# Optimization experiments

Measured on AMD Instinct MI355X. Metric: run time of the kernel, lower is better.

## Reference

```python
import jax, jax.numpy as jnp
import numpy as np

K = 32
TEMPERATURE = 0.1
RTOL, ATOL = 1e-5, 1e-5


def _embed(x, W1, b1, W2, b2, W3, b3):
    h = jax.nn.gelu(x @ W1.T + b1, approximate=False)
    h = jax.nn.gelu(h @ W2.T + b2, approximate=False)
    return jax.nn.sigmoid(h @ W3.T + b3)


def setup_inputs() -> dict:
    key = jax.random.key(0)
    ks = jax.random.split(key, 9)
    Q, N, D_IN, D_E = 256, 16384, 256, 64
    s = lambda fan_in: 1.0 / np.sqrt(fan_in)
    return {
        "x": jax.random.normal(ks[0], (Q, D_IN), jnp.float32),
        "support_x": jax.random.normal(ks[1], (N, D_IN), jnp.float32),
        "support_labels": jax.random.uniform(ks[2], (N, 1), jnp.float32),
        "W1": jax.random.normal(ks[3], (D_E, D_IN), jnp.float32) * s(D_IN),
        "b1": jax.random.normal(ks[4], (D_E,), jnp.float32) * s(D_IN),
        "W2": jax.random.normal(ks[5], (D_E, D_E), jnp.float32) * s(D_E),
        "b2": jax.random.normal(ks[6], (D_E,), jnp.float32) * s(D_E),
        "W3": jax.random.normal(ks[7], (D_E, D_E), jnp.float32) * s(D_E),
        "b3": jax.random.normal(ks[8], (D_E,), jnp.float32) * s(D_E),
    }


def reference(x, support_x, support_labels, W1, b1, W2, b2, W3, b3):
    # query embeddings [Q, D]; support embeddings [N, D] (set_support is no_grad)
    q = _embed(x, W1, b1, W2, b2, W3, b3)
    s = jax.lax.stop_gradient(_embed(support_x, W1, b1, W2, b2, W3, b3))
    # torch.cdist p=2 via expanded squared distances
    d2 = (jnp.sum(q * q, -1)[:, None] + jnp.sum(s * s, -1)[None, :]
          - 2.0 * (q @ s.T))
    dist = jnp.sqrt(jnp.maximum(d2, 0.0))  # [Q, N]
    # isclose mask: |q - s| <= atol + rtol*|s|, all over feature dim
    close = jnp.abs(q[:, None, :] - s[None, :, :]) <= (ATOL + RTOL * jnp.abs(s)[None, :, :])
    mask = jnp.all(close, axis=-1)  # [Q, N]
    dist = jnp.where(mask, jnp.inf, dist)
    # top-k smallest distances
    neg_top, idx = jax.lax.top_k(-dist, K)  # [Q, K]
    topd = -neg_top
    neighbor_labels = support_labels[idx].squeeze(-1)  # [Q, K]
    weights = jax.nn.softmax(-topd / TEMPERATURE, axis=1)
    return jnp.sum(weights * neighbor_labels, axis=1)  # [Q]
```

## Files before the change

kernel.cpp:

```cpp
#include <hip/hip_runtime.h>
#include <math.h>

#define D_IN   256
#define D_E    64
#define N_SUP  16384
#define NQ     256
#define KSEL   32
#define RTOLC  1e-5f
#define ATOLC  1e-5f
#define INV_T  10.0f

#define CHUNK  1024
#define NCH    16
#define QG     16
#define NQG    16

typedef unsigned long long ull;

__device__ __forceinline__ float gelu_exact(float x) {
    return 0.5f * x * (1.0f + erff(x * 0.70710678118654752440f));
}

__global__ __launch_bounds__(256, 2) void embed_kernel(
    const float* __restrict__ sx, const float* __restrict__ x,
    const float* __restrict__ W1, const float* __restrict__ b1,
    const float* __restrict__ W2, const float* __restrict__ b2,
    const float* __restrict__ W3, const float* __restrict__ b3,
    float* __restrict__ s_emb, float* __restrict__ s_norm,
    float* __restrict__ q_emb, float* __restrict__ q_norm)
{
    __shared__ float xc[2][64][68];
    __shared__ float wc[2][64][68];
    __shared__ float nsq[64][17];

    const int tid = threadIdx.x;
    const int rg  = tid >> 4;
    const int fg  = tid & 15;
    const bool isq = blockIdx.x >= (N_SUP / 64);
    const int rowbase = isq ? (int)(blockIdx.x - N_SUP / 64) * 64
                            : (int)blockIdx.x * 64;
    const float* src = (isq ? x : sx) + (size_t)rowbase * D_IN;

    #define STAGE_X(kc_, b_)                                                   \
        {                                                                      \
            _Pragma("unroll")                                                  \
            for (int i_ = 0; i_ < 4; ++i_) {                                   \
                int g_ = i_ * 256 + tid;                                       \
                int row_ = g_ >> 4, c4_ = g_ & 15;                             \
                float4 v_ = *reinterpret_cast<const float4*>(                  \
                    src + (size_t)row_ * D_IN + (kc_) * 64 + c4_ * 4);         \
                xc[b_][c4_ * 4 + 0][row_] = v_.x;                              \
                xc[b_][c4_ * 4 + 1][row_] = v_.y;                              \
                xc[b_][c4_ * 4 + 2][row_] = v_.z;                              \
                xc[b_][c4_ * 4 + 3][row_] = v_.w;                              \
            }                                                                  \
        }
    #define STAGE_W1(kc_, b_)                                                  \
        {                                                                      \
            _Pragma("unroll")                                                  \
            for (int i_ = 0; i_ < 4; ++i_) {                                   \
                int g_ = i_ * 256 + tid;                                       \
                int f_ = g_ >> 4, c4_ = g_ & 15;                               \
                float4 w_ = *reinterpret_cast<const float4*>(                  \
                    W1 + (size_t)f_ * D_IN + (kc_) * 64 + c4_ * 4);            \
                wc[b_][c4_ * 4 + 0][f_] = w_.x;                                \
                wc[b_][c4_ * 4 + 1][f_] = w_.y;                                \
                wc[b_][c4_ * 4 + 2][f_] = w_.z;                                \
                wc[b_][c4_ * 4 + 3][f_] = w_.w;                                \
            }                                                                  \
        }
    #define STAGE_WSQ(Wp_, b_)                                                 \
        {                                                                      \
            _Pragma("unroll")                                                  \
            for (int i_ = 0; i_ < 4; ++i_) {                                   \
                int g_ = i_ * 256 + tid;                                       \
                int f_ = g_ >> 4, c4_ = g_ & 15;                               \
                float4 w_ = *reinterpret_cast<const float4*>(                  \
                    (Wp_) + (size_t)f_ * D_E + c4_ * 4);                       \
                wc[b_][c4_ * 4 + 0][f_] = w_.x;                                \
                wc[b_][c4_ * 4 + 1][f_] = w_.y;                                \
                wc[b_][c4_ * 4 + 2][f_] = w_.z;                                \
                wc[b_][c4_ * 4 + 3][f_] = w_.w;                                \
            }                                                                  \
        }
    #define GEMM64(XB_, WB_, ACC_)                                             \
        {                                                                      \
            _Pragma("unroll 8")                                                \
            for (int k_ = 0; k_ < 64; ++k_) {                                  \
                float4 xv_ = *reinterpret_cast<const float4*>(&XB_[k_][rg * 4]); \
                float4 wv_ = *reinterpret_cast<const float4*>(&WB_[k_][fg * 4]); \
                ACC_[0][0] = fmaf(wv_.x, xv_.x, ACC_[0][0]);                   \
                ACC_[0][1] = fmaf(wv_.y, xv_.x, ACC_[0][1]);                   \
                ACC_[0][2] = fmaf(wv_.z, xv_.x, ACC_[0][2]);                   \
                ACC_[0][3] = fmaf(wv_.w, xv_.x, ACC_[0][3]);                   \
                ACC_[1][0] = fmaf(wv_.x, xv_.y, ACC_[1][0]);                   \
                ACC_[1][1] = fmaf(wv_.y, xv_.y, ACC_[1][1]);                   \
                ACC_[1][2] = fmaf(wv_.z, xv_.y, ACC_[1][2]);                   \
                ACC_[1][3] = fmaf(wv_.w, xv_.y, ACC_[1][3]);                   \
                ACC_[2][0] = fmaf(wv_.x, xv_.z, ACC_[2][0]);                   \
                ACC_[2][1] = fmaf(wv_.y, xv_.z, ACC_[2][1]);                   \
                ACC_[2][2] = fmaf(wv_.z, xv_.z, ACC_[2][2]);                   \
                ACC_[2][3] = fmaf(wv_.w, xv_.z, ACC_[2][3]);                   \
                ACC_[3][0] = fmaf(wv_.x, xv_.w, ACC_[3][0]);                   \
                ACC_[3][1] = fmaf(wv_.y, xv_.w, ACC_[3][1]);                   \
                ACC_[3][2] = fmaf(wv_.z, xv_.w, ACC_[3][2]);                   \
                ACC_[3][3] = fmaf(wv_.w, xv_.w, ACC_[3][3]);                   \
            }                                                                  \
        }

    float4 bv1 = *reinterpret_cast<const float4*>(b1 + fg * 4);
    float acc[4][4];
    #pragma unroll
    for (int j = 0; j < 4; ++j) {
        acc[j][0] = bv1.x; acc[j][1] = bv1.y; acc[j][2] = bv1.z; acc[j][3] = bv1.w;
    }
    STAGE_X(0, 0); STAGE_W1(0, 0);
    __syncthreads();
    #pragma unroll
    for (int kc = 0; kc < 4; ++kc) {
        const int b = kc & 1;
        if (kc < 3) { STAGE_X(kc + 1, b ^ 1); STAGE_W1(kc + 1, b ^ 1); }
        GEMM64(xc[b], wc[b], acc);
        __syncthreads();
    }

    #pragma unroll
    for (int j = 0; j < 4; ++j)
        #pragma unroll
        for (int i = 0; i < 4; ++i)
            xc[0][fg * 4 + i][rg * 4 + j] = gelu_exact(acc[j][i]);
    STAGE_WSQ(W2, 0);
    STAGE_WSQ(W3, 1);
    __syncthreads();

    float4 bv2 = *reinterpret_cast<const float4*>(b2 + fg * 4);
    float a2[4][4];
    #pragma unroll
    for (int j = 0; j < 4; ++j) {
        a2[j][0] = bv2.x; a2[j][1] = bv2.y; a2[j][2] = bv2.z; a2[j][3] = bv2.w;
    }
    GEMM64(xc[0], wc[0], a2);
    __syncthreads();
    #pragma unroll
    for (int j = 0; j < 4; ++j)
        #pragma unroll
        for (int i = 0; i < 4; ++i)
            xc[1][fg * 4 + i][rg * 4 + j] = gelu_exact(a2[j][i]);
    __syncthreads();

    float4 bv3 = *reinterpret_cast<const float4*>(b3 + fg * 4);
    float a3[4][4];
    #pragma unroll
    for (int j = 0; j < 4; ++j) {
        a3[j][0] = bv3.x; a3[j][1] = bv3.y; a3[j][2] = bv3.z; a3[j][3] = bv3.w;
    }
    GEMM64(xc[1], wc[1], a3);

    float* E   = isq ? q_emb  : s_emb;
    float* Nrm = isq ? q_norm : s_norm;
    #pragma unroll
    for (int j = 0; j < 4; ++j) {
        float e0 = 1.0f / (1.0f + expf(-a3[j][0]));
        float e1 = 1.0f / (1.0f + expf(-a3[j][1]));
        float e2 = 1.0f / (1.0f + expf(-a3[j][2]));
        float e3 = 1.0f / (1.0f + expf(-a3[j][3]));
        *reinterpret_cast<float4*>(E + (size_t)(rowbase + rg * 4 + j) * D_E + fg * 4)
            = make_float4(e0, e1, e2, e3);
        a3[j][0] = fmaf(e0, e0, fmaf(e1, e1, fmaf(e2, e2, e3 * e3)));
    }
    __syncthreads();
    #pragma unroll
    for (int j = 0; j < 4; ++j) nsq[rg * 4 + j][fg] = a3[j][0];
    __syncthreads();
    if (tid < 64) {
        float s = 0.0f;
        #pragma unroll
        for (int g = 0; g < 16; ++g) s += nsq[tid][g];
        Nrm[rowbase + tid] = s;
    }
    #undef STAGE_X
    #undef STAGE_W1
    #undef STAGE_WSQ
    #undef GEMM64
}

__global__ __launch_bounds__(512, 1) void knn_phaseA(
    const float* __restrict__ s_emb, const float* __restrict__ s_norm,
    const float* __restrict__ q_emb, const float* __restrict__ q_norm,
    const float* __restrict__ labels, ull* __restrict__ cand)
{
    __shared__ float tile[2][64 * 68];
    __shared__ ull   win_l[QG][KSEL];

    const int tid  = threadIdx.x;
    const int lane = tid & 63;
    const int wid  = tid >> 6;
    const int qg   = blockIdx.x >> 4;
    const int sc   = blockIdx.x & 15;
    const int qiu  = __builtin_amdgcn_readfirstlane(qg * QG + 2 * wid);
    const float* q0 = q_emb + (size_t)qiu * D_E;
    const float* q1 = q0 + D_E;
    const float  qn0 = q_norm[qiu];
    const float  qn1 = q_norm[qiu + 1];

    #pragma unroll
    for (int i = 0; i < 2; ++i) {
        int g = i * 512 + tid;
        int row = g >> 4, c4 = g & 15;
        float4 v = *reinterpret_cast<const float4*>(
            s_emb + (size_t)(sc * CHUNK + row) * D_E + c4 * 4);
        *reinterpret_cast<float4*>(&tile[0][row * 68 + c4 * 4]) = v;
    }
    __syncthreads();

    float d2a[16], d2b[16];
    #pragma unroll
    for (int s = 0; s < 16; ++s) {
        const int b = s & 1;
        float4 p0, p1;
        if (s < 15) {
            p0 = *reinterpret_cast<const float4*>(
                s_emb + (size_t)(sc * CHUNK + (s + 1) * 64 + (tid >> 4)) * D_E + (tid & 15) * 4);
            p1 = *reinterpret_cast<const float4*>(
                s_emb + (size_t)(sc * CHUNK + (s + 1) * 64 + ((512 + tid) >> 4)) * D_E + (tid & 15) * 4);
        }
        const float* tr = &tile[b][lane * 68];
        float a0 = 0.0f, a1 = 0.0f;
        #pragma unroll
        for (int c = 0; c < 16; ++c) {
            float4 sv = *reinterpret_cast<const float4*>(tr + c * 4);
            a0 = fmaf(q0[c * 4 + 0], sv.x, a0);
            a0 = fmaf(q0[c * 4 + 1], sv.y, a0);
            a0 = fmaf(q0[c * 4 + 2], sv.z, a0);
            a0 = fmaf(q0[c * 4 + 3], sv.w, a0);
            a1 = fmaf(q1[c * 4 + 0], sv.x, a1);
            a1 = fmaf(q1[c * 4 + 1], sv.y, a1);
            a1 = fmaf(q1[c * 4 + 2], sv.z, a1);
            a1 = fmaf(q1[c * 4 + 3], sv.w, a1);
        }
        const int grow = sc * CHUNK + s * 64 + lane;
        const float sn = s_norm[grow];
        float d20 = fmaxf(qn0 + sn - 2.0f * a0, 0.0f);
        float d21 = fmaxf(qn1 + sn - 2.0f * a1, 0.0f);
        if (d20 < 1e-3f) {
            bool close = true;
            for (int k = 0; k < D_E; ++k) {
                float svk = tr[k];
                close = close && (fabsf(q0[k] - svk) <= (ATOLC + RTOLC * fabsf(svk)));
            }
            if (close) d20 = INFINITY;
        }
        if (d21 < 1e-3f) {
            bool close = true;
            for (int k = 0; k < D_E; ++k) {
                float svk = tr[k];
                close = close && (fabsf(q1[k] - svk) <= (ATOLC + RTOLC * fabsf(svk)));
            }
            if (close) d21 = INFINITY;
        }
        d2a[s] = d20;
        d2b[s] = d21;
        if (s < 15) {
            *reinterpret_cast<float4*>(&tile[b ^ 1][(tid >> 4) * 68 + (tid & 15) * 4]) = p0;
            *reinterpret_cast<float4*>(&tile[b ^ 1][((512 + tid) >> 4) * 68 + (tid & 15) * 4]) = p1;
        }
        __syncthreads();
    }

    #pragma unroll
    for (int h = 0; h < 2; ++h) {
        ull sk[16];
        #pragma unroll
        for (int j = 0; j < 16; ++j) {
            float d2 = h ? d2b[j] : d2a[j];
            sk[j] = ((ull)__float_as_uint(d2) << 10) | (unsigned)(j * 64 + lane);
        }
        #pragma unroll
        for (int k = 2; k <= 16; k <<= 1) {
            #pragma unroll
            for (int j = k >> 1; j > 0; j >>= 1) {
                #pragma unroll
                for (int i = 0; i < 16; ++i) {
                    int ixj = i ^ j;
                    if (ixj > i) {
                        ull a_ = sk[i], b_ = sk[ixj];
                        bool up = (i & k) == 0;
                        bool c_ = up ? (b_ < a_) : (a_ < b_);
                        sk[i] = c_ ? b_ : a_; sk[ixj] = c_ ? a_ : b_;
                    }
                }
            }
        }
        ull lkey = sk[0];
        for (int it = 0; it < KSEL; ++it) {
            unsigned lv = (unsigned)(lkey >> 10);
            unsigned m = lv;
            #pragma unroll
            for (int off = 1; off < 64; off <<= 1) {
                unsigned o = __shfl_xor(m, off);
                m = o < m ? o : m;
            }
            ull tb = __ballot(lv == m);
            if (__popcll(tb) > 1) {
                unsigned rr = (lv == m) ? (unsigned)(lkey & 1023u) : 0xffffffffu;
                unsigned rm = rr;
                #pragma unroll
                for (int off = 1; off < 64; off <<= 1) {
                    unsigned o = __shfl_xor(rm, off);
                    rm = o < rm ? o : rm;
                }
                tb = __ballot(rr == rm);
            }
            const int wl = (int)(__ffsll((long long)tb) - 1);
            if (lane == wl) {
                win_l[2 * wid + h][it] = lkey;
                #pragma unroll
                for (int j = 0; j < 15; ++j) sk[j] = sk[j + 1];
                sk[15] = ~0ull;
                lkey = sk[0];
            }
        }
    }

    {
        const int h = lane >> 5;
        const int e = lane & 31;
        ull m = win_l[2 * wid + h][e];
        unsigned gidx = (unsigned)(sc * CHUNK) + (unsigned)(m & 1023u);
        float lab = labels[gidx];
        ull* dst = cand + ((size_t)(qiu + h) * NCH + sc) * KSEL;
        dst[e] = ((ull)(unsigned)(m >> 10) << 32) | (ull)__float_as_uint(lab);
    }
}

__global__ __launch_bounds__(256) void knn_phaseB(
    const ull* __restrict__ cand, float* __restrict__ out)
{
    const int lane = threadIdx.x & 63;
    const int wid  = threadIdx.x >> 6;
    const int q    = blockIdx.x * 4 + wid;

    const bool act = lane < NCH;
    const ull* lst = cand + ((size_t)q * NCH + (lane & 15)) * KSEL;
    int ptr = 0;
    ull cur = act ? lst[0] : ~0ull;

    float d0 = 0.0f, sw = 0.0f, sl = 0.0f;
    for (int it = 0; it < KSEL; ++it) {
        unsigned mv = (unsigned)(cur >> 32);
        unsigned ml = (unsigned)cur;
        #pragma unroll
        for (int off = 1; off < 16; off <<= 1) {
            unsigned ov = __shfl_xor(mv, off);
            unsigned ol = __shfl_xor(ml, off);
            bool take = (ov < mv) || (ov == mv && (lane & off));
            mv = take ? ov : mv;
            ml = take ? ol : ml;
        }
        ull b = __ballot(act && (unsigned)(cur >> 32) == mv);
        int wl = (int)(__ffsll((long long)b) - 1);
        if (lane == wl) {
            ++ptr;
            cur = (ptr < KSEL) ? lst[ptr] : ~0ull;
        }
        if (lane == 0) {
            float d = sqrtf(__uint_as_float(mv));
            if (it == 0) d0 = d;
            float w = expf((d0 - d) * INV_T);
            sw += w;
            sl += w * __uint_as_float(ml);
        }
    }
    if (lane == 0) out[q] = sl / sw;
}

extern "C" void kernel_launch(void* const* d_in, const int* in_sizes, int n_in,
                              void* d_out, int out_size, void* d_ws, size_t ws_size,
                              hipStream_t stream) {
    const float* x      = (const float*)d_in[0];
    const float* sx     = (const float*)d_in[1];
    const float* labels = (const float*)d_in[2];
    const float* W1     = (const float*)d_in[3];
    const float* b1     = (const float*)d_in[4];
    const float* W2     = (const float*)d_in[5];
    const float* b2     = (const float*)d_in[6];
    const float* W3     = (const float*)d_in[7];
    const float* b3     = (const float*)d_in[8];
    float* out = (float*)d_out;

    float* ws     = (float*)d_ws;
    float* s_emb  = ws;
    float* s_norm = s_emb + (size_t)N_SUP * D_E;
    float* q_emb  = s_norm + N_SUP;
    float* q_norm = q_emb + (size_t)NQ * D_E;
    ull*   cand   = (ull*)(q_norm + NQ);

    embed_kernel<<<(N_SUP + NQ) / 64, 256, 0, stream>>>(
        sx, x, W1, b1, W2, b2, W3, b3, s_emb, s_norm, q_emb, q_norm);
    knn_phaseA<<<NQG * NCH, 512, 0, stream>>>(s_emb, s_norm, q_emb, q_norm,
                                              labels, cand);
    knn_phaseB<<<NQ / 4, 256, 0, stream>>>(cand, out);
}
```

Before: 101.3 us.

## Halve embed and kNN chunk sizes and select top-k on 32-lane half-waves

The embedding kernel now uses 32-row blocks of 128 threads, giving twice as many blocks, and two barriers are removed. The kNN phase A splits the support set into 32 chunks of 512 instead of 16 of 1024. Both queries' candidates are exchanged across the wave halves so each 32-lane half selects top-k for one query at the same time, where before the two queries were handled one after the other across the full wave. Phase B merges 32 candidate lists per query instead of 16. The aim is more parallelism and a shorter serial top-k selection. The cost is more candidate traffic and more merge work in phase B, and the removed barriers may introduce shared-memory hazards.

```diff
diff --git a/kernel.cpp b/kernel.cpp
--- a/kernel.cpp
+++ b/kernel.cpp
@@ -10,8 +10,8 @@
 #define ATOLC  1e-5f
 #define INV_T  10.0f
 
-#define CHUNK  1024
-#define NCH    16
+#define CHUNK  512
+#define NCH    32
 #define QG     16
 #define NQG    16
 
@@ -21,7 +21,7 @@
     return 0.5f * x * (1.0f + erff(x * 0.70710678118654752440f));
 }
 
-__global__ __launch_bounds__(256, 2) void embed_kernel(
+__global__ __launch_bounds__(128) void embed_kernel(
     const float* __restrict__ sx, const float* __restrict__ x,
     const float* __restrict__ W1, const float* __restrict__ b1,
     const float* __restrict__ W2, const float* __restrict__ b2,
@@ -29,23 +29,23 @@
     float* __restrict__ s_emb, float* __restrict__ s_norm,
     float* __restrict__ q_emb, float* __restrict__ q_norm)
 {
-    __shared__ float xc[2][64][68];
+    __shared__ float xc[2][64][36];
     __shared__ float wc[2][64][68];
-    __shared__ float nsq[64][17];
+    __shared__ float nsq[32][17];
 
     const int tid = threadIdx.x;
     const int rg  = tid >> 4;
     const int fg  = tid & 15;
-    const bool isq = blockIdx.x >= (N_SUP / 64);
-    const int rowbase = isq ? (int)(blockIdx.x - N_SUP / 64) * 64
-                            : (int)blockIdx.x * 64;
+    const bool isq = blockIdx.x >= (N_SUP / 32);
+    const int rowbase = isq ? (int)(blockIdx.x - N_SUP / 32) * 32
+                            : (int)blockIdx.x * 32;
     const float* src = (isq ? x : sx) + (size_t)rowbase * D_IN;
 
     #define STAGE_X(kc_, b_)                                                   \
         {                                                                      \
             _Pragma("unroll")                                                  \
             for (int i_ = 0; i_ < 4; ++i_) {                                   \
-                int g_ = i_ * 256 + tid;                                       \
+                int g_ = i_ * 128 + tid;                                       \
                 int row_ = g_ >> 4, c4_ = g_ & 15;                             \
                 float4 v_ = *reinterpret_cast<const float4*>(                  \
                     src + (size_t)row_ * D_IN + (kc_) * 64 + c4_ * 4);         \
@@ -58,8 +58,8 @@
     #define STAGE_W1(kc_, b_)                                                  \
         {                                                                      \
             _Pragma("unroll")                                                  \
-            for (int i_ = 0; i_ < 4; ++i_) {                                   \
-                int g_ = i_ * 256 + tid;                                       \
+            for (int i_ = 0; i_ < 8; ++i_) {                                   \
+                int g_ = i_ * 128 + tid;                                       \
                 int f_ = g_ >> 4, c4_ = g_ & 15;                               \
                 float4 w_ = *reinterpret_cast<const float4*>(                  \
                     W1 + (size_t)f_ * D_IN + (kc_) * 64 + c4_ * 4);            \
@@ -72,8 +72,8 @@
     #define STAGE_WSQ(Wp_, b_)                                                 \
         {                                                                      \
             _Pragma("unroll")                                                  \
-            for (int i_ = 0; i_ < 4; ++i_) {                                   \
-                int g_ = i_ * 256 + tid;                                       \
+            for (int i_ = 0; i_ < 8; ++i_) {                                   \
+                int g_ = i_ * 128 + tid;                                       \
                 int f_ = g_ >> 4, c4_ = g_ & 15;                               \
                 float4 w_ = *reinterpret_cast<const float4*>(                  \
                     (Wp_) + (size_t)f_ * D_E + c4_ * 4);                       \
@@ -140,7 +140,6 @@
         a2[j][0] = bv2.x; a2[j][1] = bv2.y; a2[j][2] = bv2.z; a2[j][3] = bv2.w;
     }
     GEMM64(xc[0], wc[0], a2);
-    __syncthreads();
     #pragma unroll
     for (int j = 0; j < 4; ++j)
         #pragma unroll
@@ -168,11 +167,10 @@
             = make_float4(e0, e1, e2, e3);
         a3[j][0] = fmaf(e0, e0, fmaf(e1, e1, fmaf(e2, e2, e3 * e3)));
     }
-    __syncthreads();
     #pragma unroll
     for (int j = 0; j < 4; ++j) nsq[rg * 4 + j][fg] = a3[j][0];
     __syncthreads();
-    if (tid < 64) {
+    if (tid < 32) {
         float s = 0.0f;
         #pragma unroll
         for (int g = 0; g < 16; ++g) s += nsq[tid][g];
@@ -195,8 +193,8 @@
     const int tid  = threadIdx.x;
     const int lane = tid & 63;
     const int wid  = tid >> 6;
-    const int qg   = blockIdx.x >> 4;
-    const int sc   = blockIdx.x & 15;
+    const int qg   = blockIdx.x >> 5;
+    const int sc   = blockIdx.x & 31;
     const int qiu  = __builtin_amdgcn_readfirstlane(qg * QG + 2 * wid);
     const float* q0 = q_emb + (size_t)qiu * D_E;
     const float* q1 = q0 + D_E;
@@ -213,12 +211,12 @@
     }
     __syncthreads();
 
-    float d2a[16], d2b[16];
-    #pragma unroll
-    for (int s = 0; s < 16; ++s) {
+    float d2a[8], d2b[8];
+    #pragma unroll
+    for (int s = 0; s < 8; ++s) {
         const int b = s & 1;
         float4 p0, p1;
-        if (s < 15) {
+        if (s < 7) {
             p0 = *reinterpret_cast<const float4*>(
                 s_emb + (size_t)(sc * CHUNK + (s + 1) * 64 + (tid >> 4)) * D_E + (tid & 15) * 4);
             p1 = *reinterpret_cast<const float4*>(
@@ -260,76 +258,83 @@
         }
         d2a[s] = d20;
         d2b[s] = d21;
-        if (s < 15) {
+        if (s < 7) {
             *reinterpret_cast<float4*>(&tile[b ^ 1][(tid >> 4) * 68 + (tid & 15) * 4]) = p0;
             *reinterpret_cast<float4*>(&tile[b ^ 1][((512 + tid) >> 4) * 68 + (tid & 15) * 4]) = p1;
         }
         __syncthreads();
     }
 
-    #pragma unroll
-    for (int h = 0; h < 2; ++h) {
-        ull sk[16];
-        #pragma unroll
-        for (int j = 0; j < 16; ++j) {
-            float d2 = h ? d2b[j] : d2a[j];
-            sk[j] = ((ull)__float_as_uint(d2) << 10) | (unsigned)(j * 64 + lane);
-        }
-        #pragma unroll
-        for (int k = 2; k <= 16; k <<= 1) {
+    const int h  = lane >> 5;
+    const unsigned l5 = lane & 31;
+    ull sk[16];
+    #pragma unroll
+    for (int j = 0; j < 8; ++j) {
+        float ta  = __shfl_xor(d2a[j], 32);
+        float tbx = __shfl_xor(d2b[j], 32);
+        float vlo = h ? tbx : d2a[j];
+        float vhi = h ? d2b[j] : ta;
+        unsigned rlo = (unsigned)(j * 64) + l5;
+        sk[j]     = ((ull)__float_as_uint(vlo) << 9) | rlo;
+        sk[j + 8] = ((ull)__float_as_uint(vhi) << 9) | (rlo + 32);
+    }
+
+    #pragma unroll
+    for (int k = 2; k <= 16; k <<= 1) {
+        #pragma unroll
+        for (int j = k >> 1; j > 0; j >>= 1) {
             #pragma unroll
-            for (int j = k >> 1; j > 0; j >>= 1) {
-                #pragma unroll
-                for (int i = 0; i < 16; ++i) {
-                    int ixj = i ^ j;
-                    if (ixj > i) {
-                        ull a_ = sk[i], b_ = sk[ixj];
-                        bool up = (i & k) == 0;
-                        bool c_ = up ? (b_ < a_) : (a_ < b_);
-                        sk[i] = c_ ? b_ : a_; sk[ixj] = c_ ? a_ : b_;
-                    }
+            for (int i = 0; i < 16; ++i) {
+                int ixj = i ^ j;
+                if (ixj > i) {
+                    ull a_ = sk[i], b_ = sk[ixj];
+                    bool up = (i & k) == 0;
+                    bool c_ = up ? (b_ < a_) : (a_ < b_);
+                    sk[i] = c_ ? b_ : a_; sk[ixj] = c_ ? a_ : b_;
                 }
             }
         }
-        ull lkey = sk[0];
-        for (int it = 0; it < KSEL; ++it) {
-            unsigned lv = (unsigned)(lkey >> 10);
-            unsigned m = lv;
+    }
+
+    ull lkey = sk[0];
+    for (int it = 0; it < KSEL; ++it) {
+        unsigned lv = (unsigned)(lkey >> 9);
+        unsigned m = lv;
+        #pragma unroll
+        for (int off = 1; off < 32; off <<= 1) {
+            unsigned o = __shfl_xor(m, off);
+            m = o < m ? o : m;
+        }
+        ull tb = __ballot(lv == m);
+        bool cond;
+        if (__popcll(tb) != 2) {
+            unsigned rr = (lv == m) ? (unsigned)(lkey & 511u) : 0xffffffffu;
+            unsigned rm = rr;
             #pragma unroll
-            for (int off = 1; off < 64; off <<= 1) {
-                unsigned o = __shfl_xor(m, off);
-                m = o < m ? o : m;
+            for (int off = 1; off < 32; off <<= 1) {
+                unsigned o = __shfl_xor(rm, off);
+                rm = o < rm ? o : rm;
             }
-            ull tb = __ballot(lv == m);
-            if (__popcll(tb) > 1) {
-                unsigned rr = (lv == m) ? (unsigned)(lkey & 1023u) : 0xffffffffu;
-                unsigned rm = rr;
-                #pragma unroll
-                for (int off = 1; off < 64; off <<= 1) {
-                    unsigned o = __shfl_xor(rm, off);
-                    rm = o < rm ? o : rm;
-                }
-                tb = __ballot(rr == rm);
-            }
-            const int wl = (int)(__ffsll((long long)tb) - 1);
-            if (lane == wl) {
-                win_l[2 * wid + h][it] = lkey;
-                #pragma unroll
-                for (int j = 0; j < 15; ++j) sk[j] = sk[j + 1];
-                sk[15] = ~0ull;
-                lkey = sk[0];
-            }
+            cond = (lv == m) && ((unsigned)(lkey & 511u) == rm);
+        } else {
+            cond = (lv == m);
+        }
+        if (cond) {
+            win_l[2 * wid + h][it] = lkey;
+            #pragma unroll
+            for (int j = 0; j < 15; ++j) sk[j] = sk[j + 1];
+            sk[15] = ~0ull;
+            lkey = sk[0];
         }
     }
 
     {
-        const int h = lane >> 5;
-        const int e = lane & 31;
+        const int e = (int)l5;
         ull m = win_l[2 * wid + h][e];
-        unsigned gidx = (unsigned)(sc * CHUNK) + (unsigned)(m & 1023u);
+        unsigned gidx = (unsigned)(sc * CHUNK) + (unsigned)(m & 511u);
         float lab = labels[gidx];
-        ull* dst = cand + ((size_t)(qiu + h) * NCH + sc) * KSEL;
-        dst[e] = ((ull)(unsigned)(m >> 10) << 32) | (ull)__float_as_uint(lab);
+        ull* dst = cand + ((size_t)(qg * QG + 2 * wid + h) * NCH + sc) * KSEL;
+        dst[e] = ((ull)(unsigned)(m >> 9) << 32) | (ull)__float_as_uint(lab);
     }
 }
 
@@ -341,7 +346,7 @@
     const int q    = blockIdx.x * 4 + wid;
 
     const bool act = lane < NCH;
-    const ull* lst = cand + ((size_t)q * NCH + (lane & 15)) * KSEL;
+    const ull* lst = cand + ((size_t)q * NCH + (lane & 31)) * KSEL;
     int ptr = 0;
     ull cur = act ? lst[0] : ~0ull;
 
@@ -350,15 +355,15 @@
         unsigned mv = (unsigned)(cur >> 32);
         unsigned ml = (unsigned)cur;
         #pragma unroll
-        for (int off = 1; off < 16; off <<= 1) {
+        for (int off = 1; off < 32; off <<= 1) {
             unsigned ov = __shfl_xor(mv, off);
             unsigned ol = __shfl_xor(ml, off);
             bool take = (ov < mv) || (ov == mv && (lane & off));
             mv = take ? ov : mv;
             ml = take ? ol : ml;
         }
-        ull b = __ballot(act && (unsigned)(cur >> 32) == mv);
-        int wl = (int)(__ffsll((long long)b) - 1);
+        ull bl = __ballot(act && (unsigned)(cur >> 32) == mv);
+        int wl = (int)(__ffsll((long long)bl) - 1);
         if (lane == wl) {
             ++ptr;
             cur = (ptr < KSEL) ? lst[ptr] : ~0ull;
@@ -395,7 +400,7 @@
     float* q_norm = q_emb + (size_t)NQ * D_E;
     ull*   cand   = (ull*)(q_norm + NQ);
 
-    embed_kernel<<<(N_SUP + NQ) / 64, 256, 0, stream>>>(
+    embed_kernel<<<(N_SUP + NQ) / 32, 128, 0, stream>>>(
         sx, x, W1, b1, W2, b2, W3, b3, s_emb, s_norm, q_emb, q_norm);
     knn_phaseA<<<NQG * NCH, 512, 0, stream>>>(s_emb, s_norm, q_emb, q_norm,
                                               labels, cand);
```

New measurement: 102.9 us. Within noise of the previous version (+1.6%).
